# Kernel tuning notes

Measured on AMD Instinct MI355X. Metric: run time of the kernel, lower is better.

Reference implementation:

```python
import jax, jax.numpy as jnp
import numpy as np

N, E = 50000, 800000
IN, MID, OUT = 128, 256, 128
LN_EPS = 1e-5


def layer_norm(x, gamma, beta, eps=LN_EPS):
    mu = jnp.mean(x, axis=-1, keepdims=True)
    var = jnp.mean(jnp.square(x - mu), axis=-1, keepdims=True)
    return (x - mu) * jax.lax.rsqrt(var + eps) * gamma + beta


def gcn_conv(x, W, b, src, dst, norm, n):
    # x' = D^{-1/2}(A+I)D^{-1/2} X W + b  (self-loops already folded into src/dst/norm)
    h = x @ W                                  # [N, F_out]
    msg = h[src] * norm[:, None]               # [E+N, F_out] gather + scale
    out = jax.ops.segment_sum(msg, dst, num_segments=n)
    return out + b


def setup_inputs() -> dict:
    key = jax.random.key(0)
    ks = jax.random.split(key, 4)
    x = jax.random.normal(ks[0], (N, IN), dtype=jnp.float32)
    edge_index = jax.random.randint(ks[1], (2, E), 0, N, dtype=jnp.int32)
    W1 = jax.random.normal(ks[2], (IN, MID), dtype=jnp.float32) * (1.0 / np.sqrt(IN))
    b1 = jnp.zeros((MID,), jnp.float32)
    g1 = jnp.ones((IN,), jnp.float32)
    be1 = jnp.zeros((IN,), jnp.float32)
    W4 = jax.random.normal(ks[3], (MID, OUT), dtype=jnp.float32) * (1.0 / np.sqrt(MID))
    b4 = jnp.zeros((OUT,), jnp.float32)
    g4 = jnp.ones((MID,), jnp.float32)
    be4 = jnp.zeros((MID,), jnp.float32)
    return {"x": x, "W1": W1, "b1": b1, "g1": g1, "be1": be1,
            "W4": W4, "b4": b4, "g4": g4, "be4": be4,
            "edge_index": edge_index}


def reference(x, W1, b1, g1, be1, W4, b4, g4, be4, edge_index):
    n = x.shape[0]
    loop = jnp.arange(n, dtype=edge_index.dtype)
    src = jnp.concatenate([edge_index[0], loop])   # [E+N]
    dst = jnp.concatenate([edge_index[1], loop])   # [E+N]
    deg = jax.ops.segment_sum(jnp.ones_like(src, x.dtype), dst, num_segments=n)
    dinv = jax.lax.rsqrt(deg)                      # deg >= 1 thanks to self-loops
    norm = dinv[src] * dinv[dst]                   # [E+N]

    h = gcn_conv(layer_norm(x, g1, be1), W1, b1, src, dst, norm, n)
    h = jax.nn.gelu(h, approximate=False)          # torch F.gelu default = exact erf
    h = gcn_conv(layer_norm(h, g4, be4), W4, b4, src, dst, norm, n)
    return h
```

## Files before the change

kernel.cpp:

```cpp
#include <hip/hip_runtime.h>
#include <math.h>

#define N_NODES 50000
#define E_EDGES 800000

typedef __attribute__((ext_vector_type(4))) float f32x4;
typedef __attribute__((ext_vector_type(8))) short s16x8;

#define T1_OFF    0UL
#define A1H_OFF   12800000UL
#define A1L_OFF   25600000UL
#define T2B_OFF   38400000UL
#define WB1H_OFF  64000000UL
#define WB1L_OFF  64100096UL
#define WB4H_OFF  64200192UL
#define WB4L_OFF  64300288UL
#define DINV_OFF  64400384UL
#define HIST8_OFF 64600384UL
#define RP8_OFF   66200384UL
#define POSREL_OFF 67800448UL
#define CSRS_OFF  71000448UL
#define BSUM_OFF  74200448UL

__device__ __forceinline__ float lo16f(unsigned u) { return __uint_as_float(u << 16); }
__device__ __forceinline__ float hi16f(unsigned u) { return __uint_as_float(u & 0xffff0000u); }
__device__ __forceinline__ unsigned pack2bf(float a, float b) {
  unsigned ua = __float_as_uint(a); ua += 0x7fffu + ((ua >> 16) & 1u);
  unsigned ub = __float_as_uint(b); ub += 0x7fffu + ((ub >> 16) & 1u);
  return (ua >> 16) | (ub & 0xffff0000u);
}
__device__ __forceinline__ float gelu_f(float x) {
  return 0.5f * x * (1.f + erff(x * 0.70710678118654752f));
}

__global__ __launch_bounds__(256) void zero_hist8(int4* __restrict__ h) {
  int i = blockIdx.x * 256 + threadIdx.x;
  if (i < 100000) h[i] = make_int4(0, 0, 0, 0);
}

__global__ __launch_bounds__(256) void edge_pos(const int* __restrict__ dst,
                                                int* __restrict__ hist8,
                                                int* __restrict__ posrel) {
  int e = blockIdx.x * 256 + threadIdx.x;
  int d = dst[e];
  int seg = blockIdx.x & 7;
  int r = atomicAdd(&hist8[d * 8 + seg], 1);
  __builtin_nontemporal_store(r, posrel + e);
}

__global__ __launch_bounds__(1024) void scan_partial(const int* __restrict__ hist,
                                                     int* __restrict__ rp,
                                                     int* __restrict__ bsum,
                                                     float* __restrict__ dinv, int n) {
  __shared__ int wsum[16];
  int tid = threadIdx.x, lane = tid & 63, wv = tid >> 6;
  int i = blockIdx.x * 1024 + tid;
  int v = (i < n) ? hist[i] : 0;
  int s8 = v;
  #pragma unroll
  for (int m = 1; m < 8; m <<= 1) s8 += __shfl_xor(s8, m);
  if ((i & 7) == 0 && i < n) dinv[i >> 3] = rsqrtf((float)(s8 + 1));
  int sc = v;
  #pragma unroll
  for (int m = 1; m < 64; m <<= 1) { int o = __shfl_up(sc, m); if (lane >= m) sc += o; }
  if (lane == 63) wsum[wv] = sc;
  __syncthreads();
  if (wv == 0) {
    int w = (lane < 16) ? wsum[lane] : 0;
    int swc = w;
    #pragma unroll
    for (int m = 1; m < 16; m <<= 1) { int o = __shfl_up(swc, m); if (lane >= m) swc += o; }
    if (lane < 16) wsum[lane] = swc - w;
    if (lane == 15) bsum[blockIdx.x] = swc;
  }
  __syncthreads();
  if (i < n) rp[i] = (sc - v) + wsum[wv];
}

__global__ __launch_bounds__(64) void scan_bsums(int* __restrict__ bsum, int nb) {
  int lane = threadIdx.x;
  int carry = 0;
  for (int base = 0; base < nb; base += 64) {
    int i = base + lane;
    int v = (i < nb) ? bsum[i] : 0;
    int sc = v;
    #pragma unroll
    for (int m = 1; m < 64; m <<= 1) { int o = __shfl_up(sc, m); if (lane >= m) sc += o; }
    if (i < nb) bsum[i] = carry + sc - v;
    carry += __shfl(sc, 63);
  }
  if (lane == 0) bsum[nb] = carry;
}

__global__ __launch_bounds__(1024) void scan_add(int* __restrict__ rp,
                                                 const int* __restrict__ bsum, int n) {
  int i = blockIdx.x * 1024 + threadIdx.x;
  if (i < n) rp[i] += bsum[blockIdx.x];
  if (i == 0) rp[n] = bsum[gridDim.x];
}

__global__ __launch_bounds__(256) void fill2(const int* __restrict__ src,
                                             const int* __restrict__ dst,
                                             const int* __restrict__ rp8,
                                             const int* __restrict__ posrel,
                                             unsigned short* __restrict__ csr_src) {
  int e = blockIdx.x * 256 + threadIdx.x;
  int s = src[e], d = dst[e];
  int seg = blockIdx.x & 7;
  int pos = rp8[d * 8 + seg] + posrel[e];
  __builtin_nontemporal_store((unsigned short)s, csr_src + pos);
}

__device__ __forceinline__ void convW_body(const float* __restrict__ W,
                                           unsigned* __restrict__ Wh,
                                           unsigned* __restrict__ Wl,
                                           int K, int N, int tid) {
  if (tid >= (K * N) / 8) return;
  int c15 = tid & 15;
  int kg  = (tid >> 4) & 3;
  int KS  = K >> 5;
  int ks  = (tid >> 6) % KS;
  int nt  = (tid >> 6) / KS;
  int col = nt * 16 + c15;
  int k0  = ks * 32 + kg * 8;
  float w[8];
  #pragma unroll
  for (int j = 0; j < 8; ++j) w[j] = W[(size_t)(k0 + j) * N + col];
  uint4 h, l;
  h.x = pack2bf(w[0], w[1]); l.x = pack2bf(w[0] - lo16f(h.x), w[1] - hi16f(h.x));
  h.y = pack2bf(w[2], w[3]); l.y = pack2bf(w[2] - lo16f(h.y), w[3] - hi16f(h.y));
  h.z = pack2bf(w[4], w[5]); l.z = pack2bf(w[4] - lo16f(h.z), w[5] - hi16f(h.z));
  h.w = pack2bf(w[6], w[7]); l.w = pack2bf(w[6] - lo16f(h.w), w[7] - hi16f(h.w));
  *reinterpret_cast<uint4*>(Wh + (size_t)tid * 4) = h;
  *reinterpret_cast<uint4*>(Wl + (size_t)tid * 4) = l;
}

__global__ __launch_bounds__(256) void convW_both(const float* __restrict__ W1,
                                                  const float* __restrict__ W4,
                                                  unsigned* __restrict__ Wh1,
                                                  unsigned* __restrict__ Wl1,
                                                  unsigned* __restrict__ Wh4,
                                                  unsigned* __restrict__ Wl4) {
  int b = blockIdx.x;
  if (b < 16) convW_body(W1, Wh1, Wl1, 128, 256, b * 256 + threadIdx.x);
  else        convW_body(W4, Wh4, Wl4, 256, 128, (b - 16) * 256 + threadIdx.x);
}

__global__ __launch_bounds__(256) void ln1_kernel(const float* __restrict__ x,
                                                  const float* __restrict__ g,
                                                  const float* __restrict__ be,
                                                  unsigned* __restrict__ T) {
  int lane = threadIdx.x & 63, wv = threadIdx.x >> 6;
  int row = blockIdx.x * 4 + wv;
  float2 v = *reinterpret_cast<const float2*>(x + (size_t)row * 128 + lane * 2);
  float s = v.x + v.y, sq = v.x * v.x + v.y * v.y;
  #pragma unroll
  for (int m = 1; m < 64; m <<= 1) { s += __shfl_xor(s, m); sq += __shfl_xor(sq, m); }
  float mu = s * (1.f / 128.f);
  float var = sq * (1.f / 128.f) - mu * mu;
  float rs = rsqrtf(var + 1e-5f);
  float2 gg = *reinterpret_cast<const float2*>(g + lane * 2);
  float2 bb = *reinterpret_cast<const float2*>(be + lane * 2);
  T[(size_t)row * 64 + lane] =
      pack2bf((v.x - mu) * rs * gg.x + bb.x, (v.y - mu) * rs * gg.y + bb.y);
}

template <int MODE>
__global__ __launch_bounds__(256) void agg128(const unsigned* __restrict__ T,
                                              const int* __restrict__ rp8,
                                              const unsigned short* __restrict__ csr,
                                              const float* __restrict__ dinv,
                                              const float* __restrict__ b,
                                              float* __restrict__ out,
                                              unsigned* __restrict__ outh,
                                              unsigned* __restrict__ outl) {
  int lane = threadIdx.x & 63, wv = threadIdx.x >> 6;
  int node = blockIdx.x * 4 + wv;
  float di = dinv[node], sn = di * di;
  unsigned us = T[(size_t)node * 64 + lane];
  float a0 = lo16f(us) * sn, a1 = hi16f(us) * sn;
  float b0 = 0.f, b1 = 0.f;
  int e = rp8[node * 8], e1 = rp8[node * 8 + 8];
  if (e + 7 < e1) {
    int sA[8];
    #pragma unroll
    for (int j = 0; j < 8; ++j) sA[j] = csr[e + j];
    for (;;) {
      unsigned u[8];
      float nn[8];
      #pragma unroll
      for (int j = 0; j < 8; ++j) u[j] = T[(size_t)sA[j] * 64 + lane];
      #pragma unroll
      for (int j = 0; j < 8; ++j) nn[j] = dinv[sA[j]];
      e += 8;
      bool more = (e + 7 < e1);
      int sB[8];
      if (more) {
        #pragma unroll
        for (int j = 0; j < 8; ++j) sB[j] = csr[e + j];
      }
      #pragma unroll
      for (int j = 0; j < 8; ++j) {
        float nr = nn[j] * di;
        if (j & 1) { b0 += lo16f(u[j]) * nr; b1 += hi16f(u[j]) * nr; }
        else       { a0 += lo16f(u[j]) * nr; a1 += hi16f(u[j]) * nr; }
      }
      if (!more) break;
      #pragma unroll
      for (int j = 0; j < 8; ++j) sA[j] = sB[j];
    }
  }
  for (; e < e1; ++e) {
    int s = csr[e];
    unsigned u = T[(size_t)s * 64 + lane];
    float nr = dinv[s] * di;
    a0 += lo16f(u) * nr; a1 += hi16f(u) * nr;
  }
  a0 += b0; a1 += b1;
  if (MODE == 0) {
    unsigned h = pack2bf(a0, a1);
    float r0 = a0 - lo16f(h), r1 = a1 - hi16f(h);
    outh[(size_t)node * 64 + lane] = h;
    outl[(size_t)node * 64 + lane] = pack2bf(r0, r1);
  } else {
    float2 bb = *reinterpret_cast<const float2*>(b + lane * 2);
    *reinterpret_cast<float2*>(out + (size_t)node * 128 + lane * 2) =
        make_float2(a0 + bb.x, a1 + bb.y);
  }
}

__global__ __launch_bounds__(256) void gemm1_fused(const unsigned* __restrict__ Ah,
                                                   const unsigned* __restrict__ Al,
                                                   const unsigned* __restrict__ Wh,
                                                   const unsigned* __restrict__ Wl,
                                                   const float* __restrict__ b,
                                                   const float* __restrict__ g,
                                                   const float* __restrict__ be,
                                                   unsigned* __restrict__ T2b, int n) {
  __shared__ float st[32 * 260];
  int t = threadIdx.x, lane = t & 63, w = t >> 6;
  int kg = lane >> 4, c15 = lane & 15;
  int c0 = w * 64;
  int row0 = blockIdx.x * 32 + c15;
  int r0 = min(row0, n - 1);
  int r1 = min(row0 + 16, n - 1);
  const unsigned* ah0 = Ah + (size_t)r0 * 64 + kg * 4;
  const unsigned* al0 = Al + (size_t)r0 * 64 + kg * 4;
  const unsigned* ah1 = Ah + (size_t)r1 * 64 + kg * 4;
  const unsigned* al1 = Al + (size_t)r1 * 64 + kg * 4;
  f32x4 acc[2][4];
  #pragma unroll
  for (int rt = 0; rt < 2; ++rt)
    #pragma unroll
    for (int nf = 0; nf < 4; ++nf) acc[rt][nf] = (f32x4)(0.f);
  #pragma unroll
  for (int ks = 0; ks < 4; ++ks) {
    s16x8 bh[4], bl[4];
    #pragma unroll
    for (int nf = 0; nf < 4; ++nf) {
      int nt = (c0 >> 4) + nf;
      size_t bo = (size_t)(((nt * 4 + ks) * 4 + kg) * 16 + c15) * 4;
      bh[nf] = *reinterpret_cast<const s16x8*>(Wh + bo);
      bl[nf] = *reinterpret_cast<const s16x8*>(Wl + bo);
    }
    s16x8 a0h = *reinterpret_cast<const s16x8*>(ah0 + ks * 16);
    s16x8 a0l = *reinterpret_cast<const s16x8*>(al0 + ks * 16);
    s16x8 a1h = *reinterpret_cast<const s16x8*>(ah1 + ks * 16);
    s16x8 a1l = *reinterpret_cast<const s16x8*>(al1 + ks * 16);
    #pragma unroll
    for (int nf = 0; nf < 4; ++nf) {
      acc[0][nf] = __builtin_amdgcn_mfma_f32_16x16x32_bf16(a0h, bh[nf], acc[0][nf], 0, 0, 0);
      acc[0][nf] = __builtin_amdgcn_mfma_f32_16x16x32_bf16(a0l, bh[nf], acc[0][nf], 0, 0, 0);
      acc[0][nf] = __builtin_amdgcn_mfma_f32_16x16x32_bf16(a0h, bl[nf], acc[0][nf], 0, 0, 0);
      acc[1][nf] = __builtin_amdgcn_mfma_f32_16x16x32_bf16(a1h, bh[nf], acc[1][nf], 0, 0, 0);
      acc[1][nf] = __builtin_amdgcn_mfma_f32_16x16x32_bf16(a1l, bh[nf], acc[1][nf], 0, 0, 0);
      acc[1][nf] = __builtin_amdgcn_mfma_f32_16x16x32_bf16(a1h, bl[nf], acc[1][nf], 0, 0, 0);
    }
  }
  #pragma unroll
  for (int rt = 0; rt < 2; ++rt)
    #pragma unroll
    for (int nf = 0; nf < 4; ++nf) {
      int col = c0 + nf * 16 + c15;
      float bb = b[col];
      #pragma unroll
      for (int r = 0; r < 4; ++r) {
        int row = rt * 16 + kg * 4 + r;
        st[row * 260 + col] = gelu_f(acc[rt][nf][r] + bb);
      }
    }
  __syncthreads();
  float4 gg = *reinterpret_cast<const float4*>(g + lane * 4);
  float4 bb2 = *reinterpret_cast<const float4*>(be + lane * 4);
  #pragma unroll
  for (int rr = 0; rr < 8; ++rr) {
    int row = w * 8 + rr;
    float4 v = *reinterpret_cast<const float4*>(&st[row * 260 + lane * 4]);
    float s = v.x + v.y + v.z + v.w;
    float sq = v.x * v.x + v.y * v.y + v.z * v.z + v.w * v.w;
    #pragma unroll
    for (int m = 1; m < 64; m <<= 1) { s += __shfl_xor(s, m); sq += __shfl_xor(sq, m); }
    float mu = s * (1.f / 256.f);
    float var = sq * (1.f / 256.f) - mu * mu;
    float rs = rsqrtf(var + 1e-5f);
    int gr = blockIdx.x * 32 + row;
    if (gr < n) {
      uint2 p;
      p.x = pack2bf((v.x - mu) * rs * gg.x + bb2.x, (v.y - mu) * rs * gg.y + bb2.y);
      p.y = pack2bf((v.z - mu) * rs * gg.z + bb2.z, (v.w - mu) * rs * gg.w + bb2.w);
      *reinterpret_cast<uint2*>(T2b + (size_t)gr * 128 + lane * 2) = p;
    }
  }
}

__global__ __launch_bounds__(256) void gemm2_mfma(const unsigned* __restrict__ Ab,
                                                  const unsigned* __restrict__ Wh,
                                                  const unsigned* __restrict__ Wl,
                                                  unsigned* __restrict__ T2, int n) {
  __shared__ float st[32 * 132];
  int t = threadIdx.x, lane = t & 63, w = t >> 6;
  int kg = lane >> 4, c15 = lane & 15;
  int c0 = w * 32;
  int row0 = blockIdx.x * 32 + c15;
  int r0 = min(row0, n - 1);
  int r1 = min(row0 + 16, n - 1);
  const unsigned* ap0 = Ab + (size_t)r0 * 128 + kg * 4;
  const unsigned* ap1 = Ab + (size_t)r1 * 128 + kg * 4;
  f32x4 acc[2][2];
  #pragma unroll
  for (int rt = 0; rt < 2; ++rt) { acc[rt][0] = (f32x4)(0.f); acc[rt][1] = (f32x4)(0.f); }
  #pragma unroll
  for (int ks = 0; ks < 8; ++ks) {
    s16x8 bh[2], bl[2];
    #pragma unroll
    for (int nf = 0; nf < 2; ++nf) {
      int nt = (c0 >> 4) + nf;
      size_t bo = (size_t)(((nt * 8 + ks) * 4 + kg) * 16 + c15) * 4;
      bh[nf] = *reinterpret_cast<const s16x8*>(Wh + bo);
      bl[nf] = *reinterpret_cast<const s16x8*>(Wl + bo);
    }
    s16x8 a0 = *reinterpret_cast<const s16x8*>(ap0 + ks * 16);
    s16x8 a1 = *reinterpret_cast<const s16x8*>(ap1 + ks * 16);
    #pragma unroll
    for (int nf = 0; nf < 2; ++nf) {
      acc[0][nf] = __builtin_amdgcn_mfma_f32_16x16x32_bf16(a0, bh[nf], acc[0][nf], 0, 0, 0);
      acc[0][nf] = __builtin_amdgcn_mfma_f32_16x16x32_bf16(a0, bl[nf], acc[0][nf], 0, 0, 0);
      acc[1][nf] = __builtin_amdgcn_mfma_f32_16x16x32_bf16(a1, bh[nf], acc[1][nf], 0, 0, 0);
      acc[1][nf] = __builtin_amdgcn_mfma_f32_16x16x32_bf16(a1, bl[nf], acc[1][nf], 0, 0, 0);
    }
  }
  #pragma unroll
  for (int rt = 0; rt < 2; ++rt)
    #pragma unroll
    for (int nf = 0; nf < 2; ++nf) {
      int col = c0 + nf * 16 + c15;
      #pragma unroll
      for (int r = 0; r < 4; ++r) {
        int row = rt * 16 + kg * 4 + r;
        st[row * 132 + col] = acc[rt][nf][r];
      }
    }
  __syncthreads();
  #pragma unroll
  for (int rr = 0; rr < 8; ++rr) {
    int row = w * 8 + rr;
    int gr = blockIdx.x * 32 + row;
    if (gr < n) {
      float2 v = *reinterpret_cast<const float2*>(&st[row * 132 + lane * 2]);
      T2[(size_t)gr * 64 + lane] = pack2bf(v.x, v.y);
    }
  }
}

extern "C" void kernel_launch(void* const* d_in, const int* in_sizes, int n_in,
                              void* d_out, int out_size, void* d_ws, size_t ws_size,
                              hipStream_t stream) {
  (void)in_sizes; (void)n_in; (void)out_size; (void)ws_size;
  const float* x   = (const float*)d_in[0];
  const float* W1  = (const float*)d_in[1];
  const float* b1  = (const float*)d_in[2];
  const float* g1  = (const float*)d_in[3];
  const float* be1 = (const float*)d_in[4];
  const float* W4  = (const float*)d_in[5];
  const float* b4  = (const float*)d_in[6];
  const float* g4  = (const float*)d_in[7];
  const float* be4 = (const float*)d_in[8];
  const int*   ei  = (const int*)d_in[9];
  const int* src = ei;
  const int* dst = ei + E_EDGES;

  char* ws = (char*)d_ws;
  unsigned* T1    = (unsigned*)(ws + T1_OFF);
  unsigned* T2    = (unsigned*)(ws + T1_OFF);
  unsigned* A1h   = (unsigned*)(ws + A1H_OFF);
  unsigned* A1l   = (unsigned*)(ws + A1L_OFF);
  unsigned* T2b   = (unsigned*)(ws + T2B_OFF);
  unsigned* Wb1h  = (unsigned*)(ws + WB1H_OFF);
  unsigned* Wb1l  = (unsigned*)(ws + WB1L_OFF);
  unsigned* Wb4h  = (unsigned*)(ws + WB4H_OFF);
  unsigned* Wb4l  = (unsigned*)(ws + WB4L_OFF);
  float* dinv     = (float*)(ws + DINV_OFF);
  int*   hist8    = (int*)(ws + HIST8_OFF);
  int*   rp8      = (int*)(ws + RP8_OFF);
  int*   posrel   = (int*)(ws + POSREL_OFF);
  unsigned short* csr_src = (unsigned short*)(ws + CSRS_OFF);
  int*   bsum     = (int*)(ws + BSUM_OFF);
  float* outp     = (float*)d_out;

  const int NSEG = N_NODES * 8;
  int nblkE  = E_EDGES / 256;
  int nbScan = (NSEG + 1023) / 1024;
  int nblkG  = (N_NODES + 31) / 32;

  hipLaunchKernelGGL(zero_hist8, dim3(391), dim3(256), 0, stream, (int4*)hist8);
  hipLaunchKernelGGL(edge_pos, dim3(nblkE), dim3(256), 0, stream, dst, hist8, posrel);
  hipLaunchKernelGGL(scan_partial, dim3(nbScan), dim3(1024), 0, stream,
                     hist8, rp8, bsum, dinv, NSEG);
  hipLaunchKernelGGL(scan_bsums, dim3(1), dim3(64), 0, stream, bsum, nbScan);
  hipLaunchKernelGGL(scan_add, dim3(nbScan), dim3(1024), 0, stream, rp8, bsum, NSEG);
  hipLaunchKernelGGL(fill2, dim3(nblkE), dim3(256), 0, stream, src, dst, rp8, posrel, csr_src);
  hipLaunchKernelGGL(convW_both, dim3(32), dim3(256), 0, stream,
                     W1, W4, Wb1h, Wb1l, Wb4h, Wb4l);

  hipLaunchKernelGGL(ln1_kernel, dim3(N_NODES / 4), dim3(256), 0, stream, x, g1, be1, T1);
  hipLaunchKernelGGL(agg128<0>, dim3(N_NODES / 4), dim3(256), 0, stream,
                     T1, rp8, csr_src, dinv, (const float*)nullptr,
                     (float*)nullptr, A1h, A1l);
  hipLaunchKernelGGL(gemm1_fused, dim3(nblkG), dim3(256), 0, stream,
                     A1h, A1l, Wb1h, Wb1l, b1, g4, be4, T2b, N_NODES);

  hipLaunchKernelGGL(gemm2_mfma, dim3(nblkG), dim3(256), 0, stream, T2b, Wb4h, Wb4l, T2, N_NODES);
  hipLaunchKernelGGL(agg128<2>, dim3(N_NODES / 4), dim3(256), 0, stream,
                     T2, rp8, csr_src, dinv, b4, outp,
                     (unsigned*)nullptr, (unsigned*)nullptr);
}
```

Baseline: 233.8 us.

## Split feature tables into column chunks and aggregate four edges per wave

The bf16 feature tables written by the LN1 and GEMM2 epilogues are stored as four column-chunk planes of 16 words (32 features) per node instead of one 64-word row. The aggregation kernel becomes agg32: each block handles one chunk for 8 nodes, and each wave processes four edges at once using 16-lane groups, then reduces them with shuffles. The aim is a smaller per-chunk working set that fits better in L2 and higher memory parallelism for the gather. The cost is that the CSR indices and dinv values are now read once per chunk (four times overall), the 8-edge software pipelining is gone, and lanes sit idle when a node's degree is not a multiple of four.

```diff
diff --git a/kernel.cpp b/kernel.cpp
--- a/kernel.cpp
+++ b/kernel.cpp
@@ -3,6 +3,7 @@
 
 #define N_NODES 50000
 #define E_EDGES 800000
+#define CHUNK_U (N_NODES * 16)
 
 typedef __attribute__((ext_vector_type(4))) float f32x4;
 typedef __attribute__((ext_vector_type(8))) short s16x8;
@@ -161,71 +162,52 @@
   float rs = rsqrtf(var + 1e-5f);
   float2 gg = *reinterpret_cast<const float2*>(g + lane * 2);
   float2 bb = *reinterpret_cast<const float2*>(be + lane * 2);
-  T[(size_t)row * 64 + lane] =
+  T[(size_t)(lane >> 4) * CHUNK_U + (size_t)row * 16 + (lane & 15)] =
       pack2bf((v.x - mu) * rs * gg.x + bb.x, (v.y - mu) * rs * gg.y + bb.y);
 }
 
 template <int MODE>
-__global__ __launch_bounds__(256) void agg128(const unsigned* __restrict__ T,
-                                              const int* __restrict__ rp8,
-                                              const unsigned short* __restrict__ csr,
-                                              const float* __restrict__ dinv,
-                                              const float* __restrict__ b,
-                                              float* __restrict__ out,
-                                              unsigned* __restrict__ outh,
-                                              unsigned* __restrict__ outl) {
-  int lane = threadIdx.x & 63, wv = threadIdx.x >> 6;
-  int node = blockIdx.x * 4 + wv;
-  float di = dinv[node], sn = di * di;
-  unsigned us = T[(size_t)node * 64 + lane];
-  float a0 = lo16f(us) * sn, a1 = hi16f(us) * sn;
-  float b0 = 0.f, b1 = 0.f;
-  int e = rp8[node * 8], e1 = rp8[node * 8 + 8];
-  if (e + 7 < e1) {
-    int sA[8];
-    #pragma unroll
-    for (int j = 0; j < 8; ++j) sA[j] = csr[e + j];
-    for (;;) {
-      unsigned u[8];
-      float nn[8];
-      #pragma unroll
-      for (int j = 0; j < 8; ++j) u[j] = T[(size_t)sA[j] * 64 + lane];
-      #pragma unroll
-      for (int j = 0; j < 8; ++j) nn[j] = dinv[sA[j]];
-      e += 8;
-      bool more = (e + 7 < e1);
-      int sB[8];
-      if (more) {
-        #pragma unroll
-        for (int j = 0; j < 8; ++j) sB[j] = csr[e + j];
-      }
-      #pragma unroll
-      for (int j = 0; j < 8; ++j) {
-        float nr = nn[j] * di;
-        if (j & 1) { b0 += lo16f(u[j]) * nr; b1 += hi16f(u[j]) * nr; }
-        else       { a0 += lo16f(u[j]) * nr; a1 += hi16f(u[j]) * nr; }
-      }
-      if (!more) break;
-      #pragma unroll
-      for (int j = 0; j < 8; ++j) sA[j] = sB[j];
-    }
-  }
-  for (; e < e1; ++e) {
-    int s = csr[e];
-    unsigned u = T[(size_t)s * 64 + lane];
-    float nr = dinv[s] * di;
+__global__ __launch_bounds__(256) void agg32(const unsigned* __restrict__ Tc,
+                                             const int* __restrict__ rp8,
+                                             const unsigned short* __restrict__ csr,
+                                             const float* __restrict__ dinv,
+                                             const float* __restrict__ b,
+                                             float* __restrict__ out,
+                                             unsigned* __restrict__ outh,
+                                             unsigned* __restrict__ outl) {
+  int t = threadIdx.x, lane = t & 63, wv = t >> 6;
+  int bid = blockIdx.x;
+  int cid = bid & 7;
+  int chunk = cid >> 1, half = cid & 1;
+  int node = (bid >> 3) * 8 + half * 4 + wv;
+  int q = lane >> 4, l16 = lane & 15;
+  const unsigned* Tch = Tc + (size_t)chunk * CHUNK_U;
+  float di = dinv[node];
+  float a0 = 0.f, a1 = 0.f;
+  int e0 = rp8[node * 8], e1 = rp8[node * 8 + 8];
+  for (int e = e0; e < e1; e += 4) {
+    int qe = e + q;
+    bool valid = qe < e1;
+    int s = csr[valid ? qe : e];
+    unsigned u = Tch[(size_t)s * 16 + l16];
+    float nr = valid ? dinv[s] * di : 0.f;
     a0 += lo16f(u) * nr; a1 += hi16f(u) * nr;
   }
-  a0 += b0; a1 += b1;
-  if (MODE == 0) {
-    unsigned h = pack2bf(a0, a1);
-    float r0 = a0 - lo16f(h), r1 = a1 - hi16f(h);
-    outh[(size_t)node * 64 + lane] = h;
-    outl[(size_t)node * 64 + lane] = pack2bf(r0, r1);
-  } else {
-    float2 bb = *reinterpret_cast<const float2*>(b + lane * 2);
-    *reinterpret_cast<float2*>(out + (size_t)node * 128 + lane * 2) =
-        make_float2(a0 + bb.x, a1 + bb.y);
+  a0 += __shfl_xor(a0, 16); a1 += __shfl_xor(a1, 16);
+  a0 += __shfl_xor(a0, 32); a1 += __shfl_xor(a1, 32);
+  if (q == 0) {
+    unsigned us = Tch[(size_t)node * 16 + l16];
+    float sn = di * di;
+    a0 += lo16f(us) * sn; a1 += hi16f(us) * sn;
+    if (MODE == 0) {
+      unsigned h = pack2bf(a0, a1);
+      outh[(size_t)node * 64 + chunk * 16 + l16] = h;
+      outl[(size_t)node * 64 + chunk * 16 + l16] = pack2bf(a0 - lo16f(h), a1 - hi16f(h));
+    } else {
+      float2 bb = *reinterpret_cast<const float2*>(b + chunk * 32 + l16 * 2);
+      *reinterpret_cast<float2*>(out + (size_t)node * 128 + chunk * 32 + l16 * 2) =
+          make_float2(a0 + bb.x, a1 + bb.y);
+    }
   }
 }
 
@@ -367,7 +349,7 @@
     int gr = blockIdx.x * 32 + row;
     if (gr < n) {
       float2 v = *reinterpret_cast<const float2*>(&st[row * 132 + lane * 2]);
-      T2[(size_t)gr * 64 + lane] = pack2bf(v.x, v.y);
+      T2[(size_t)(lane >> 4) * CHUNK_U + (size_t)gr * 16 + (lane & 15)] = pack2bf(v.x, v.y);
     }
   }
 }
@@ -411,6 +393,7 @@
   int nblkE  = E_EDGES / 256;
   int nbScan = (NSEG + 1023) / 1024;
   int nblkG  = (N_NODES + 31) / 32;
+  int nblkA  = (N_NODES / 8) * 8;
 
   hipLaunchKernelGGL(zero_hist8, dim3(391), dim3(256), 0, stream, (int4*)hist8);
   hipLaunchKernelGGL(edge_pos, dim3(nblkE), dim3(256), 0, stream, dst, hist8, posrel);
@@ -423,14 +406,14 @@
                      W1, W4, Wb1h, Wb1l, Wb4h, Wb4l);
 
   hipLaunchKernelGGL(ln1_kernel, dim3(N_NODES / 4), dim3(256), 0, stream, x, g1, be1, T1);
-  hipLaunchKernelGGL(agg128<0>, dim3(N_NODES / 4), dim3(256), 0, stream,
+  hipLaunchKernelGGL(agg32<0>, dim3(nblkA), dim3(256), 0, stream,
                      T1, rp8, csr_src, dinv, (const float*)nullptr,
                      (float*)nullptr, A1h, A1l);
   hipLaunchKernelGGL(gemm1_fused, dim3(nblkG), dim3(256), 0, stream,
                      A1h, A1l, Wb1h, Wb1l, b1, g4, be4, T2b, N_NODES);
 
   hipLaunchKernelGGL(gemm2_mfma, dim3(nblkG), dim3(256), 0, stream, T2b, Wb4h, Wb4l, T2, N_NODES);
-  hipLaunchKernelGGL(agg128<2>, dim3(N_NODES / 4), dim3(256), 0, stream,
+  hipLaunchKernelGGL(agg32<2>, dim3(nblkA), dim3(256), 0, stream,
                      T2, rp8, csr_src, dinv, b4, outp,
                      (unsigned*)nullptr, (unsigned*)nullptr);
 }
```

Result: slower. 361.6 us (+54.7%).
